# Optimization experiments

Hardware: AMD Instinct MI355X
Metric: run time of the kernel (lower is better)

## Reference

```python
import jax, jax.numpy as jnp
import numpy as np

V, D, N, K = 500000, 64, 50000, 32


def setup_inputs() -> dict:
    key = jax.random.key(0)
    ks = jax.random.split(key, 8)
    return {
        "embeddings": jax.random.normal(ks[0], (V, D), dtype=jnp.float32),
        "W1": jax.random.normal(ks[1], (2 * D, D), dtype=jnp.float32) * 0.05,
        "b1": jnp.zeros((D,), dtype=jnp.float32),
        "W2": jax.random.normal(ks[2], (D, D), dtype=jnp.float32) * 0.05,
        "b2": jnp.zeros((D,), dtype=jnp.float32),
        "w3": jax.random.normal(ks[3], (D, 1), dtype=jnp.float32) * 0.05,
        "b3": jnp.zeros((1,), dtype=jnp.float32),
        "video_nodes": jax.random.randint(ks[4], (N,), 0, V, dtype=jnp.int32),
        "neigh_idx": jax.random.randint(ks[5], (N, K), 0, V, dtype=jnp.int32),
        "neigh_deg": jax.random.randint(ks[6], (N,), 0, K + 1, dtype=jnp.int32),
    }


def reference(embeddings, W1, b1, W2, b2, w3, b3, video_nodes, neigh_idx, neigh_deg):
    # Ragged neighbor gather (padded to K, masked by degree)
    e = embeddings[neigh_idx]                      # [N, K, D] neighbor embeddings
    u = embeddings[video_nodes]                    # [N, D]    center embeddings
    # GraphRec-style attention: MLP on [neigh, center] concat -> scalar score
    x = jnp.concatenate(
        [e, jnp.broadcast_to(u[:, None, :], e.shape)], axis=-1)  # [N, K, 2D]
    h = jax.nn.relu(x @ W1 + b1)
    h = jax.nn.relu(h @ W2 + b2)
    s = (h @ w3)[..., 0] + b3[0]                   # [N, K]
    mask = jnp.arange(K)[None, :] < neigh_deg[:, None]
    s = jnp.where(mask, s, -1e9)                   # mask padded neighbors
    att = jax.nn.softmax(s, axis=-1)               # softmax over valid neighbors
    out = jnp.einsum('nkd,nk->nd', e, att)         # attention-weighted sum
    # num_neighs == 0 -> fall back to node's own embedding
    out = jnp.where((neigh_deg > 0)[:, None], out, u)
    return out
```

## Files before the change

### kernel.cpp

```cpp
#include <hip/hip_runtime.h>
#include <hip/hip_bf16.h>

typedef __bf16 bf16x8 __attribute__((ext_vector_type(8)));
typedef float  f32x4  __attribute__((ext_vector_type(4)));

#define MFMA32(acc, a, b) acc = __builtin_amdgcn_mfma_f32_16x16x32_bf16(a, b, acc, 0, 0, 0)

__device__ __forceinline__ bf16x8 cvt8(float4 a, float4 b) {
  bf16x8 r;
  r[0] = (__bf16)a.x; r[1] = (__bf16)a.y; r[2] = (__bf16)a.z; r[3] = (__bf16)a.w;
  r[4] = (__bf16)b.x; r[5] = (__bf16)b.y; r[6] = (__bf16)b.z; r[7] = (__bf16)b.w;
  return r;
}

template <int CTRL>
__device__ __forceinline__ float dpp_fadd(float x) {
  int yi = __builtin_amdgcn_update_dpp(0, __builtin_bit_cast(int, x), CTRL, 0xF, 0xF, true);
  return x + __builtin_bit_cast(float, yi);
}
template <int CTRL>
__device__ __forceinline__ float dpp_fmax(float x) {
  int yi = __builtin_amdgcn_update_dpp(0, __builtin_bit_cast(int, x), CTRL, 0xF, 0xF, true);
  return fmaxf(x, __builtin_bit_cast(float, yi));
}

__global__ void prep_frags(const float* __restrict__ W1,
                           const float* __restrict__ W2,
                           __bf16* __restrict__ wf) {
  int idx = blockIdx.x * 256 + threadIdx.x;
  if (idx < 8192) {
    int j = idx & 7, lane = (idx >> 3) & 63, mt = (idx >> 9) & 3, ks = idx >> 11;
    int i = ks * 32 + ((lane >> 4) << 3) + j;
    int col = mt * 16 + (lane & 15);
    wf[idx] = (__bf16)W1[i * 64 + col];
  } else if (idx < 12288) {
    int t = idx - 8192;
    int j = t & 7, lane = (t >> 3) & 63, mt2 = (t >> 9) & 3, ks2 = (t >> 11) & 1;
    int g = (lane >> 4) & 3;
    int rho = (ks2 * 2 + (j >> 2)) * 16 + g * 4 + (j & 3);
    wf[idx] = (__bf16)W2[rho * 64 + mt2 * 16 + (lane & 15)];
  }
}

__global__ __launch_bounds__(512) void graph_agg(
    const float* __restrict__ emb,
    const float* __restrict__ b1g,
    const float* __restrict__ b2g,
    const float* __restrict__ w3g,
    const float* __restrict__ b3g,
    const int* __restrict__ vn,
    const int* __restrict__ ni,
    const int* __restrict__ nd,
    const __bf16* __restrict__ wf,
    float* __restrict__ out,
    int N) {
  __shared__ __align__(16) unsigned char smem[25344];

  {
    const uint4* src = (const uint4*)wf;
    uint4* dst = (uint4*)smem;
#pragma unroll
    for (int i = 0; i < 3; i++) dst[threadIdx.x + i * 512] = src[threadIdx.x + i * 512];
    int t = threadIdx.x;
    if (t < 64) {
      ((float*)(smem + 24576))[t] = b1g[t];
      ((float*)(smem + 24832))[t] = b2g[t];
      ((float*)(smem + 25088))[t] = w3g[t];
    }
  }
  __syncthreads();

  const __bf16* w1f = (const __bf16*)smem;
  const __bf16* w2f = (const __bf16*)(smem + 16384);
  const int wid = threadIdx.x >> 6;
  const int l   = threadIdx.x & 63;
  const int g   = l >> 4;
  const int lr  = l & 15;
  const float b3v = b3g[0];

  const int gw = blockIdx.x * 8 + wid;
  const int nwaves = gridDim.x * 8;

  int n = gw;
  int node = 0, deg = 0, i0 = 0, i1 = 0;
  if (n < N) {
    node = vn[n]; deg = nd[n];
    i0 = ni[n * 32 + lr]; i1 = ni[n * 32 + 16 + lr];
  }

  for (; n < N; n += nwaves) {
    const int cn = node, cd = deg, ci0 = i0, ci1 = i1;
    {
      int nn = n + nwaves; if (nn >= N) nn = n;
      node = vn[nn]; deg = nd[nn];
      i0 = ni[nn * 32 + lr]; i1 = ni[nn * 32 + 16 + lr];
    }
    const float* ub = emb + (long)cn * 64;

    if (cd == 0) {
      out[(long)n * 64 + l] = ub[l];
      continue;
    }
    const bool m1 = (cd > 16);

    int boff = 24576;
    asm volatile("" : "+v"(boff));
    const unsigned char* bb = smem + boff;

    bf16x8 ef[2][2];
    bf16x8 uf[2];
    {
      const bool v = (lr < cd);
      const float* p = emb + (long)(v ? ci0 : cn) * 64 + g * 8;
      float4 a0 = *(const float4*)p,        a1 = *(const float4*)(p + 4);
      float4 c0 = *(const float4*)(p + 32), c1 = *(const float4*)(p + 36);
      if (!v) { a0 = a1 = c0 = c1 = make_float4(0.f, 0.f, 0.f, 0.f); }
      ef[0][0] = cvt8(a0, a1); ef[0][1] = cvt8(c0, c1);
    }
    if (m1) {
      const bool v = (16 + lr < cd);
      const float* p = emb + (long)(v ? ci1 : cn) * 64 + g * 8;
      float4 a0 = *(const float4*)p,        a1 = *(const float4*)(p + 4);
      float4 c0 = *(const float4*)(p + 32), c1 = *(const float4*)(p + 36);
      if (!v) { a0 = a1 = c0 = c1 = make_float4(0.f, 0.f, 0.f, 0.f); }
      ef[1][0] = cvt8(a0, a1); ef[1][1] = cvt8(c0, c1);
    }
    {
      const float* q = ub + g * 8;
      uf[0] = cvt8(*(const float4*)q,        *(const float4*)(q + 4));
      uf[1] = cvt8(*(const float4*)(q + 32), *(const float4*)(q + 36));
    }

    f32x4 acc1[4][2];
#pragma unroll
    for (int mt = 0; mt < 4; mt++) {
      f32x4 bv = *(const f32x4*)(bb + (mt * 16 + g * 4) * 4);
      acc1[mt][0] = bv; acc1[mt][1] = bv;
    }
#pragma unroll
    for (int ks = 0; ks < 4; ks++) {
      bf16x8 xb0 = (ks < 2) ? ef[0][ks] : uf[ks - 2];
#pragma unroll
      for (int mt = 0; mt < 4; mt++) {
        bf16x8 wa = *(const bf16x8*)(w1f + ((ks * 4 + mt) * 64 + l) * 8);
        MFMA32(acc1[mt][0], wa, xb0);
        if (m1) {
          bf16x8 xb1 = (ks < 2) ? ef[1][ks] : uf[ks - 2];
          MFMA32(acc1[mt][1], wa, xb1);
        }
      }
    }

    bf16x8 hb[2][2];
#pragma unroll
    for (int ks2 = 0; ks2 < 2; ks2++) {
#pragma unroll
      for (int nt = 0; nt < 2; nt++) {
        if (nt == 0 || m1) {
          bf16x8 v;
#pragma unroll
          for (int j = 0; j < 8; j++) {
            const int mt = ks2 * 2 + (j >> 2), r = j & 3;
            v[j] = (__bf16)fmaxf(acc1[mt][nt][r], 0.f);
          }
          hb[ks2][nt] = v;
        }
      }
    }

    f32x4 acc2[4][2];
#pragma unroll
    for (int mt2 = 0; mt2 < 4; mt2++) {
      f32x4 bv = *(const f32x4*)(bb + 256 + (mt2 * 16 + g * 4) * 4);
      acc2[mt2][0] = bv; acc2[mt2][1] = bv;
    }
#pragma unroll
    for (int ks2 = 0; ks2 < 2; ks2++) {
#pragma unroll
      for (int mt2 = 0; mt2 < 4; mt2++) {
        bf16x8 wa = *(const bf16x8*)(w2f + ((ks2 * 4 + mt2) * 64 + l) * 8);
        MFMA32(acc2[mt2][0], wa, hb[ks2][0]);
        if (m1) MFMA32(acc2[mt2][1], wa, hb[ks2][1]);
      }
    }

    float sv0 = 0.f, sv1 = 0.f;
    {
#pragma unroll
      for (int mt2 = 0; mt2 < 4; mt2++) {
        f32x4 wv = *(const f32x4*)(bb + 512 + (mt2 * 16 + g * 4) * 4);
#pragma unroll
        for (int r = 0; r < 4; r++) {
          sv0 += fmaxf(acc2[mt2][0][r], 0.f) * wv[r];
          if (m1) sv1 += fmaxf(acc2[mt2][1][r], 0.f) * wv[r];
        }
      }
    }
    sv0 += __shfl_xor(sv0, 16); sv0 += __shfl_xor(sv0, 32);
    if (m1) { sv1 += __shfl_xor(sv1, 16); sv1 += __shfl_xor(sv1, 32); }

    const bool v0 = (lr < cd);
    const bool v1 = m1 && (16 + lr < cd);
    sv0 = v0 ? (sv0 + b3v) : -1e30f;
    sv1 = v1 ? (sv1 + b3v) : -1e30f;

    float mx = fmaxf(sv0, sv1);
    mx = dpp_fmax<0x128>(mx);
    mx = dpp_fmax<0x124>(mx);
    mx = dpp_fmax<0x122>(mx);
    mx = dpp_fmax<0x121>(mx);

    float p0 = v0 ? __expf(sv0 - mx) : 0.f;
    float p1 = v1 ? __expf(sv1 - mx) : 0.f;
    float sum = p0 + p1;
    sum = dpp_fadd<0x128>(sum);
    sum = dpp_fadd<0x124>(sum);
    sum = dpp_fadd<0x122>(sum);
    sum = dpp_fadd<0x121>(sum);
    const float inv = 1.f / sum;
    const float a0 = p0 * inv, a1 = p1 * inv;

    float o[16];
#pragma unroll
    for (int ks = 0; ks < 2; ks++)
#pragma unroll
      for (int j = 0; j < 8; j++) {
        float v = a0 * (float)ef[0][ks][j];
        if (m1) v += a1 * (float)ef[1][ks][j];
        o[ks * 8 + j] = v;
      }
#pragma unroll
    for (int t = 0; t < 16; t++) {
      o[t] = dpp_fadd<0x118>(o[t]);
      o[t] = dpp_fadd<0x114>(o[t]);
      o[t] = dpp_fadd<0x112>(o[t]);
      o[t] = dpp_fadd<0x111>(o[t]);
    }

    if (lr == 15) {
      float* op = out + (long)n * 64;
      *(float4*)(op + g * 8)      = make_float4(o[0],  o[1],  o[2],  o[3]);
      *(float4*)(op + g * 8 + 4)  = make_float4(o[4],  o[5],  o[6],  o[7]);
      *(float4*)(op + 32 + g * 8) = make_float4(o[8],  o[9],  o[10], o[11]);
      *(float4*)(op + 36 + g * 8) = make_float4(o[12], o[13], o[14], o[15]);
    }
  }
}

extern "C" void kernel_launch(void* const* d_in, const int* in_sizes, int n_in,
                              void* d_out, int out_size, void* d_ws, size_t ws_size,
                              hipStream_t stream) {
  const float* emb = (const float*)d_in[0];
  const float* W1  = (const float*)d_in[1];
  const float* b1  = (const float*)d_in[2];
  const float* W2  = (const float*)d_in[3];
  const float* b2  = (const float*)d_in[4];
  const float* w3  = (const float*)d_in[5];
  const float* b3  = (const float*)d_in[6];
  const int* vn = (const int*)d_in[7];
  const int* ni = (const int*)d_in[8];
  const int* nd = (const int*)d_in[9];
  float* out = (float*)d_out;
  const int N = in_sizes[7];
  __bf16* wf = (__bf16*)d_ws;

  prep_frags<<<48, 256, 0, stream>>>(W1, W2, wf);
  graph_agg<<<1024, 512, 0, stream>>>(emb, b1, b2, w3, b3, vn, ni, nd, wf, out, N);
}
```

Before: 76.60 us.

## Prefetch next node's embedding rows during MLP and use transpose-style lane reduction

The embedding gathers for the next node (center row and neighbor rows) are now issued into registers before the current node's score and softmax phase, so global-load latency overlaps with compute instead of stalling at the top of each iteration. The final weighted-sum reduction across 16 lanes is replaced with a recursive-halving exchange where each lane ends up owning one output element. This replaces 64 DPP add steps with 15 and lets all lanes write output instead of one. It raises register pressure from the extra float4 prefetch registers, which may reduce occupancy at 512 threads per block.

```diff
diff --git a/kernel.cpp b/kernel.cpp
--- a/kernel.cpp
+++ b/kernel.cpp
@@ -5,6 +5,7 @@
 typedef float  f32x4  __attribute__((ext_vector_type(4)));
 
 #define MFMA32(acc, a, b) acc = __builtin_amdgcn_mfma_f32_16x16x32_bf16(a, b, acc, 0, 0, 0)
+#define LD4(p) (*(const float4*)(p))
 
 __device__ __forceinline__ bf16x8 cvt8(float4 a, float4 b) {
   bf16x8 r;
@@ -14,15 +15,14 @@
 }
 
 template <int CTRL>
-__device__ __forceinline__ float dpp_fadd(float x) {
+__device__ __forceinline__ float dpp_mov(float x) {
   int yi = __builtin_amdgcn_update_dpp(0, __builtin_bit_cast(int, x), CTRL, 0xF, 0xF, true);
-  return x + __builtin_bit_cast(float, yi);
+  return __builtin_bit_cast(float, yi);
 }
 template <int CTRL>
-__device__ __forceinline__ float dpp_fmax(float x) {
-  int yi = __builtin_amdgcn_update_dpp(0, __builtin_bit_cast(int, x), CTRL, 0xF, 0xF, true);
-  return fmaxf(x, __builtin_bit_cast(float, yi));
-}
+__device__ __forceinline__ float dpp_fadd(float x) { return x + dpp_mov<CTRL>(x); }
+template <int CTRL>
+__device__ __forceinline__ float dpp_fmax(float x) { return fmaxf(x, dpp_mov<CTRL>(x)); }
 
 __global__ void prep_frags(const float* __restrict__ W1,
                            const float* __restrict__ W2,
@@ -42,6 +42,19 @@
   }
 }
 
+#define ISSUE_RAW(XN, XD, XI0, XI1) do {                                      \
+    const float* up_ = emb + (long)(XN) * 64 + g * 8;                         \
+    ru0 = LD4(up_); ru1 = LD4(up_ + 4); ru2 = LD4(up_ + 32); ru3 = LD4(up_ + 36); \
+    const int a0_ = ((lr) < (XD)) ? (XI0) : (XN);                             \
+    const float* p0_ = emb + (long)a0_ * 64 + g * 8;                          \
+    re0a = LD4(p0_); re0b = LD4(p0_ + 4); re0c = LD4(p0_ + 32); re0d = LD4(p0_ + 36); \
+    if ((XD) > 16) {                                                          \
+      const int a1_ = (16 + (lr) < (XD)) ? (XI1) : (XN);                      \
+      const float* p1_ = emb + (long)a1_ * 64 + g * 8;                        \
+      re1a = LD4(p1_); re1b = LD4(p1_ + 4); re1c = LD4(p1_ + 32); re1d = LD4(p1_ + 36); \
+    }                                                                         \
+  } while (0)
+
 __global__ __launch_bounds__(512) void graph_agg(
     const float* __restrict__ emb,
     const float* __restrict__ b1g,
@@ -81,111 +94,112 @@
   const int gw = blockIdx.x * 8 + wid;
   const int nwaves = gridDim.x * 8;
 
+  const float4 z4 = make_float4(0.f, 0.f, 0.f, 0.f);
+  float4 ru0 = z4, ru1 = z4, ru2 = z4, ru3 = z4;
+  float4 re0a = z4, re0b = z4, re0c = z4, re0d = z4;
+  float4 re1a = z4, re1b = z4, re1c = z4, re1d = z4;
+
   int n = gw;
-  int node = 0, deg = 0, i0 = 0, i1 = 0;
+  int cd = 0;
   if (n < N) {
-    node = vn[n]; deg = nd[n];
-    i0 = ni[n * 32 + lr]; i1 = ni[n * 32 + 16 + lr];
+    const int n0 = vn[n];
+    cd = nd[n];
+    const int j0 = ni[(long)n * 32 + lr];
+    const int j1 = ni[(long)n * 32 + 16 + lr];
+    ISSUE_RAW(n0, cd, j0, j1);
   }
 
   for (; n < N; n += nwaves) {
-    const int cn = node, cd = deg, ci0 = i0, ci1 = i1;
-    {
-      int nn = n + nwaves; if (nn >= N) nn = n;
-      node = vn[nn]; deg = nd[nn];
-      i0 = ni[nn * 32 + lr]; i1 = ni[nn * 32 + 16 + lr];
-    }
-    const float* ub = emb + (long)cn * 64;
-
-    if (cd == 0) {
-      out[(long)n * 64 + l] = ub[l];
-      continue;
-    }
     const bool m1 = (cd > 16);
+
+    int nn = n + nwaves; if (nn >= N) nn = n;
+    const int xn = vn[nn], xd = nd[nn];
+    const int xi0 = ni[(long)nn * 32 + lr];
+    const int xi1 = ni[(long)nn * 32 + 16 + lr];
 
     int boff = 24576;
     asm volatile("" : "+v"(boff));
     const unsigned char* bb = smem + boff;
 
-    bf16x8 ef[2][2];
-    bf16x8 uf[2];
-    {
-      const bool v = (lr < cd);
-      const float* p = emb + (long)(v ? ci0 : cn) * 64 + g * 8;
-      float4 a0 = *(const float4*)p,        a1 = *(const float4*)(p + 4);
-      float4 c0 = *(const float4*)(p + 32), c1 = *(const float4*)(p + 36);
-      if (!v) { a0 = a1 = c0 = c1 = make_float4(0.f, 0.f, 0.f, 0.f); }
-      ef[0][0] = cvt8(a0, a1); ef[0][1] = cvt8(c0, c1);
-    }
-    if (m1) {
-      const bool v = (16 + lr < cd);
-      const float* p = emb + (long)(v ? ci1 : cn) * 64 + g * 8;
-      float4 a0 = *(const float4*)p,        a1 = *(const float4*)(p + 4);
-      float4 c0 = *(const float4*)(p + 32), c1 = *(const float4*)(p + 36);
-      if (!v) { a0 = a1 = c0 = c1 = make_float4(0.f, 0.f, 0.f, 0.f); }
-      ef[1][0] = cvt8(a0, a1); ef[1][1] = cvt8(c0, c1);
-    }
-    {
-      const float* q = ub + g * 8;
-      uf[0] = cvt8(*(const float4*)q,        *(const float4*)(q + 4));
-      uf[1] = cvt8(*(const float4*)(q + 32), *(const float4*)(q + 36));
-    }
-
-    f32x4 acc1[4][2];
-#pragma unroll
-    for (int mt = 0; mt < 4; mt++) {
-      f32x4 bv = *(const f32x4*)(bb + (mt * 16 + g * 4) * 4);
-      acc1[mt][0] = bv; acc1[mt][1] = bv;
-    }
-#pragma unroll
-    for (int ks = 0; ks < 4; ks++) {
-      bf16x8 xb0 = (ks < 2) ? ef[0][ks] : uf[ks - 2];
+    if (cd == 0) {
+      if (lr == 0) {
+        float* op = out + (long)n * 64;
+        *(float4*)(op + g * 8)      = ru0;
+        *(float4*)(op + g * 8 + 4)  = ru1;
+        *(float4*)(op + 32 + g * 8) = ru2;
+        *(float4*)(op + 36 + g * 8) = ru3;
+      }
+      ISSUE_RAW(xn, xd, xi0, xi1);
+    } else {
+      const bool v0c = (lr < cd);
+      const bool v1c = m1 && (16 + lr < cd);
+      bf16x8 ef00, ef01, ef10, ef11, uf0, uf1;
+      {
+        float4 a = v0c ? re0a : z4, b = v0c ? re0b : z4;
+        float4 c = v0c ? re0c : z4, d = v0c ? re0d : z4;
+        ef00 = cvt8(a, b); ef01 = cvt8(c, d);
+      }
+      if (m1) {
+        float4 a = v1c ? re1a : z4, b = v1c ? re1b : z4;
+        float4 c = v1c ? re1c : z4, d = v1c ? re1d : z4;
+        ef10 = cvt8(a, b); ef11 = cvt8(c, d);
+      }
+      uf0 = cvt8(ru0, ru1); uf1 = cvt8(ru2, ru3);
+
+      f32x4 acc1[4][2];
 #pragma unroll
       for (int mt = 0; mt < 4; mt++) {
-        bf16x8 wa = *(const bf16x8*)(w1f + ((ks * 4 + mt) * 64 + l) * 8);
-        MFMA32(acc1[mt][0], wa, xb0);
-        if (m1) {
-          bf16x8 xb1 = (ks < 2) ? ef[1][ks] : uf[ks - 2];
-          MFMA32(acc1[mt][1], wa, xb1);
+        f32x4 bv = *(const f32x4*)(bb + (mt * 16 + g * 4) * 4);
+        acc1[mt][0] = bv; acc1[mt][1] = bv;
+      }
+      const bf16x8 xb0s[4] = {ef00, ef01, uf0, uf1};
+      const bf16x8 xb1s[4] = {ef10, ef11, uf0, uf1};
+#pragma unroll
+      for (int ks = 0; ks < 4; ks++) {
+#pragma unroll
+        for (int mt = 0; mt < 4; mt++) {
+          bf16x8 wa = *(const bf16x8*)(w1f + ((ks * 4 + mt) * 64 + l) * 8);
+          MFMA32(acc1[mt][0], wa, xb0s[ks]);
+          if (m1) MFMA32(acc1[mt][1], wa, xb1s[ks]);
         }
       }
-    }
-
-    bf16x8 hb[2][2];
-#pragma unroll
-    for (int ks2 = 0; ks2 < 2; ks2++) {
-#pragma unroll
-      for (int nt = 0; nt < 2; nt++) {
-        if (nt == 0 || m1) {
-          bf16x8 v;
-#pragma unroll
-          for (int j = 0; j < 8; j++) {
-            const int mt = ks2 * 2 + (j >> 2), r = j & 3;
-            v[j] = (__bf16)fmaxf(acc1[mt][nt][r], 0.f);
+
+      bf16x8 hb[2][2];
+#pragma unroll
+      for (int ks2 = 0; ks2 < 2; ks2++) {
+#pragma unroll
+        for (int nt = 0; nt < 2; nt++) {
+          if (nt == 0 || m1) {
+            bf16x8 v;
+#pragma unroll
+            for (int j = 0; j < 8; j++) {
+              const int mt = ks2 * 2 + (j >> 2), r = j & 3;
+              v[j] = (__bf16)fmaxf(acc1[mt][nt][r], 0.f);
+            }
+            hb[ks2][nt] = v;
           }
-          hb[ks2][nt] = v;
         }
       }
-    }
-
-    f32x4 acc2[4][2];
-#pragma unroll
-    for (int mt2 = 0; mt2 < 4; mt2++) {
-      f32x4 bv = *(const f32x4*)(bb + 256 + (mt2 * 16 + g * 4) * 4);
-      acc2[mt2][0] = bv; acc2[mt2][1] = bv;
-    }
-#pragma unroll
-    for (int ks2 = 0; ks2 < 2; ks2++) {
+
+      f32x4 acc2[4][2];
 #pragma unroll
       for (int mt2 = 0; mt2 < 4; mt2++) {
-        bf16x8 wa = *(const bf16x8*)(w2f + ((ks2 * 4 + mt2) * 64 + l) * 8);
-        MFMA32(acc2[mt2][0], wa, hb[ks2][0]);
-        if (m1) MFMA32(acc2[mt2][1], wa, hb[ks2][1]);
-      }
-    }
-
-    float sv0 = 0.f, sv1 = 0.f;
-    {
+        f32x4 bv = *(const f32x4*)(bb + 256 + (mt2 * 16 + g * 4) * 4);
+        acc2[mt2][0] = bv; acc2[mt2][1] = bv;
+      }
+#pragma unroll
+      for (int ks2 = 0; ks2 < 2; ks2++) {
+#pragma unroll
+        for (int mt2 = 0; mt2 < 4; mt2++) {
+          bf16x8 wa = *(const bf16x8*)(w2f + ((ks2 * 4 + mt2) * 64 + l) * 8);
+          MFMA32(acc2[mt2][0], wa, hb[ks2][0]);
+          if (m1) MFMA32(acc2[mt2][1], wa, hb[ks2][1]);
+        }
+      }
+
+      ISSUE_RAW(xn, xd, xi0, xi1);
+
+      float sv0 = 0.f, sv1 = 0.f;
 #pragma unroll
       for (int mt2 = 0; mt2 < 4; mt2++) {
         f32x4 wv = *(const f32x4*)(bb + 512 + (mt2 * 16 + g * 4) * 4);
@@ -195,55 +209,74 @@
           if (m1) sv1 += fmaxf(acc2[mt2][1][r], 0.f) * wv[r];
         }
       }
+      sv0 += __shfl_xor(sv0, 16); sv0 += __shfl_xor(sv0, 32);
+      if (m1) { sv1 += __shfl_xor(sv1, 16); sv1 += __shfl_xor(sv1, 32); }
+
+      const bool w0 = (lr < cd);
+      const bool w1v = m1 && (16 + lr < cd);
+      sv0 = w0 ? (sv0 + b3v) : -1e30f;
+      sv1 = w1v ? (sv1 + b3v) : -1e30f;
+
+      float mx = fmaxf(sv0, sv1);
+      mx = dpp_fmax<0x128>(mx);
+      mx = dpp_fmax<0x124>(mx);
+      mx = dpp_fmax<0x122>(mx);
+      mx = dpp_fmax<0x121>(mx);
+
+      float p0 = w0 ? __expf(sv0 - mx) : 0.f;
+      float p1 = w1v ? __expf(sv1 - mx) : 0.f;
+      float sum = p0 + p1;
+      sum = dpp_fadd<0x128>(sum);
+      sum = dpp_fadd<0x124>(sum);
+      sum = dpp_fadd<0x122>(sum);
+      sum = dpp_fadd<0x121>(sum);
+      const float inv = 1.f / sum;
+      const float a0 = p0 * inv, a1 = p1 * inv;
+
+      float o[16];
+#pragma unroll
+      for (int j = 0; j < 8; j++) {
+        float v = a0 * (float)ef00[j];
+        if (m1) v += a1 * (float)ef10[j];
+        o[j] = v;
+        float w = a0 * (float)ef01[j];
+        if (m1) w += a1 * (float)ef11[j];
+        o[8 + j] = w;
+      }
+      float q8[8];
+#pragma unroll
+      for (int t = 0; t < 8; t++) {
+        const bool up = (lr & 8);
+        float sel = up ? o[t + 8] : o[t];
+        float oth = up ? o[t] : o[t + 8];
+        q8[t] = sel + dpp_mov<0x128>(oth);
+      }
+      float q4[4];
+#pragma unroll
+      for (int t = 0; t < 4; t++) {
+        const bool up = (lr & 4);
+        float sel = up ? q8[t + 4] : q8[t];
+        float oth = up ? q8[t] : q8[t + 4];
+        q4[t] = sel + __shfl_xor(oth, 4);
+      }
+      float q2[2];
+#pragma unroll
+      for (int t = 0; t < 2; t++) {
+        const bool up = (lr & 2);
+        float sel = up ? q4[t + 2] : q4[t];
+        float oth = up ? q4[t] : q4[t + 2];
+        q2[t] = sel + dpp_mov<0x4E>(oth);
+      }
+      {
+        const bool up = (lr & 1);
+        float sel = up ? q2[1] : q2[0];
+        float oth = up ? q2[0] : q2[1];
+        float r = sel + dpp_mov<0xB1>(oth);
+        out[(long)n * 64 + ((lr >> 3) << 5) + g * 8 + (lr & 7)] = r;
+      }
     }
-    sv0 += __shfl_xor(sv0, 16); sv0 += __shfl_xor(sv0, 32);
-    if (m1) { sv1 += __shfl_xor(sv1, 16); sv1 += __shfl_xor(sv1, 32); }
-
-    const bool v0 = (lr < cd);
-    const bool v1 = m1 && (16 + lr < cd);
-    sv0 = v0 ? (sv0 + b3v) : -1e30f;
-    sv1 = v1 ? (sv1 + b3v) : -1e30f;
-
-    float mx = fmaxf(sv0, sv1);
-    mx = dpp_fmax<0x128>(mx);
-    mx = dpp_fmax<0x124>(mx);
-    mx = dpp_fmax<0x122>(mx);
-    mx = dpp_fmax<0x121>(mx);
-
-    float p0 = v0 ? __expf(sv0 - mx) : 0.f;
-    float p1 = v1 ? __expf(sv1 - mx) : 0.f;
-    float sum = p0 + p1;
-    sum = dpp_fadd<0x128>(sum);
-    sum = dpp_fadd<0x124>(sum);
-    sum = dpp_fadd<0x122>(sum);
-    sum = dpp_fadd<0x121>(sum);
-    const float inv = 1.f / sum;
-    const float a0 = p0 * inv, a1 = p1 * inv;
-
-    float o[16];
-#pragma unroll
-    for (int ks = 0; ks < 2; ks++)
-#pragma unroll
-      for (int j = 0; j < 8; j++) {
-        float v = a0 * (float)ef[0][ks][j];
-        if (m1) v += a1 * (float)ef[1][ks][j];
-        o[ks * 8 + j] = v;
-      }
-#pragma unroll
-    for (int t = 0; t < 16; t++) {
-      o[t] = dpp_fadd<0x118>(o[t]);
-      o[t] = dpp_fadd<0x114>(o[t]);
-      o[t] = dpp_fadd<0x112>(o[t]);
-      o[t] = dpp_fadd<0x111>(o[t]);
-    }
-
-    if (lr == 15) {
-      float* op = out + (long)n * 64;
-      *(float4*)(op + g * 8)      = make_float4(o[0],  o[1],  o[2],  o[3]);
-      *(float4*)(op + g * 8 + 4)  = make_float4(o[4],  o[5],  o[6],  o[7]);
-      *(float4*)(op + 32 + g * 8) = make_float4(o[8],  o[9],  o[10], o[11]);
-      *(float4*)(op + 36 + g * 8) = make_float4(o[12], o[13], o[14], o[15]);
-    }
+
+    cd = xd;
   }
 }
 
```

Result: slower. 82.06 us (+7.1%).
